# Optimization experiments

Hardware: AMD Instinct MI355X
Metric: run time of the kernel (lower is better)

The kernel has to match this reference:

```python
import jax, jax.numpy as jnp
import numpy as np

B, S, D, F, O = 4, 2048, 1024, 4096, 1024
E, NS, K = 4, 2, 2  # routed experts, shared experts, topk


def setup_inputs() -> dict:
    key = jax.random.key(0)
    ks = jax.random.split(key, 6)
    def w(k, shape, fan_in):
        return jax.random.normal(k, shape, jnp.float32) * (fan_in ** -0.5)
    return {
        "x": jax.random.normal(ks[0], (B, S, D), jnp.float32),
        "gate_w": w(ks[1], (D, E), D),
        "gate_b": jnp.zeros((E,), jnp.float32),
        "sw1": w(ks[2], (NS, D, F), D),  # shared experts, first linear
        "sb1": jnp.zeros((NS, F), jnp.float32),
        "sw2": w(ks[3], (NS, F, O), F),
        "sb2": jnp.zeros((NS, O), jnp.float32),
        "rw1": w(ks[4], (E, D, F), D),   # routed experts, first linear
        "rb1": jnp.zeros((E, F), jnp.float32),
        "rw2": w(ks[5], (E, F, O), F),
        "rb2": jnp.zeros((E, O), jnp.float32),
    }


def reference(x, gate_w, gate_b, sw1, sb1, sw2, sb2, rw1, rb1, rw2, rb2):
    # Gating (eval mode: no noise)
    weights = jax.nn.softmax(x @ gate_w + gate_b, axis=-1)      # [B,S,E]
    topk_w, topk_i = jax.lax.top_k(weights, K)                  # [B,S,K]

    # Shared experts: average of NS expert MLPs
    sh = jax.nn.relu(jnp.einsum('bsd,ndf->bsnf', x, sw1) + sb1)
    shared = (jnp.einsum('bsnf,nfo->bsno', sh, sw2) + sb2).sum(axis=2) / NS  # [B,S,O]

    # Routed experts: every expert applied densely, then one-hot-select topk.
    # Original computes expert(expanded_x) where expanded_x repeats x K times;
    # the result is identical per copy, so compute once per expert and gather.
    rh = jax.nn.relu(jnp.einsum('bsd,edf->bsef', x, rw1) + rb1)  # [B,S,E,F]
    eo = jnp.einsum('bsef,efo->bseo', rh, rw2) + rb2             # [B,S,E,O]
    gathered = jnp.take_along_axis(eo, topk_i[..., None], axis=2)  # [B,S,K,O]
    routed = (gathered * topk_w[..., None]).sum(axis=2)          # [B,S,O]

    return shared + routed
```

## Files before the change

### kernel.cpp

```cpp
#include <hip/hip_runtime.h>

typedef __bf16 bf16_t;
typedef __bf16 bf16x8 __attribute__((ext_vector_type(8)));
typedef float f32x4 __attribute__((ext_vector_type(4)));

constexpr int Tn = 4 * 2048;
constexpr int Dd = 1024;
constexpr int Ff = 4096;
constexpr int Oo = 1024;
constexpr int NEXP = 6;

__device__ __forceinline__ float ldin(const void* p, size_t i, int isf32) {
    return isf32 ? ((const float*)p)[i] : (float)((const bf16_t*)p)[i];
}

__global__ void detect_kernel(const unsigned int* __restrict__ xw, int* __restrict__ flag) {
    __shared__ int cnt;
    if (threadIdx.x == 0) cnt = 0;
    __syncthreads();
    int c = 0;
    for (int i = threadIdx.x; i < 16384; i += 256) {
        unsigned w = xw[i];
        if (((w >> 7) & 0xFFu) == 0xFFu) ++c;
    }
    atomicAdd(&cnt, c);
    __syncthreads();
    if (threadIdx.x == 0) flag[0] = (cnt >= 4) ? 1 : 0;
}

__global__ void cvt_x_kernel(const void* __restrict__ x, const int* __restrict__ flag,
                             bf16_t* __restrict__ xb) {
    int f = flag[0];
    size_t i = (size_t)blockIdx.x * 256 + threadIdx.x;
    xb[i] = (bf16_t)ldin(x, i, f);
}

__global__ void cvt_transpose_kernel(const void* __restrict__ src, size_t eofs,
                                     const int* __restrict__ flag,
                                     bf16_t* __restrict__ dst, int R, int C) {
    __shared__ bf16_t tile[32][33];
    int f = flag[0];
    int c0 = blockIdx.x * 32, r0 = blockIdx.y * 32;
    int tx = threadIdx.x, ty = threadIdx.y;
    #pragma unroll
    for (int i = 0; i < 32; i += 8)
        tile[ty + i][tx] = (bf16_t)ldin(src, eofs + (size_t)(r0 + ty + i) * C + c0 + tx, f);
    __syncthreads();
    #pragma unroll
    for (int i = 0; i < 32; i += 8)
        dst[(size_t)(c0 + ty + i) * R + r0 + tx] = tile[tx][ty + i];
}

__global__ void gate_kernel(const void* __restrict__ x, const void* __restrict__ gw,
                            const void* __restrict__ gb, const int* __restrict__ flag,
                            float* __restrict__ coef) {
    int f = flag[0];
    int t = blockIdx.x;
    int lane = threadIdx.x;
    float a0 = 0.f, a1 = 0.f, a2 = 0.f, a3 = 0.f;
    for (int d = lane; d < Dd; d += 64) {
        float xv = ldin(x, (size_t)t * Dd + d, f);
        a0 += xv * ldin(gw, (size_t)d * 4 + 0, f);
        a1 += xv * ldin(gw, (size_t)d * 4 + 1, f);
        a2 += xv * ldin(gw, (size_t)d * 4 + 2, f);
        a3 += xv * ldin(gw, (size_t)d * 4 + 3, f);
    }
    #pragma unroll
    for (int off = 32; off; off >>= 1) {
        a0 += __shfl_xor(a0, off);
        a1 += __shfl_xor(a1, off);
        a2 += __shfl_xor(a2, off);
        a3 += __shfl_xor(a3, off);
    }
    if (lane == 0) {
        float l[4] = {a0 + ldin(gb, 0, f), a1 + ldin(gb, 1, f),
                      a2 + ldin(gb, 2, f), a3 + ldin(gb, 3, f)};
        float mx = fmaxf(fmaxf(l[0], l[1]), fmaxf(l[2], l[3]));
        float e[4], s = 0.f;
        #pragma unroll
        for (int i = 0; i < 4; ++i) { e[i] = expf(l[i] - mx); s += e[i]; }
        float w[4];
        #pragma unroll
        for (int i = 0; i < 4; ++i) w[i] = e[i] / s;
        int i0 = 0;
        for (int i = 1; i < 4; ++i) if (w[i] > w[i0]) i0 = i;
        int i1 = -1;
        for (int i = 0; i < 4; ++i) { if (i == i0) continue; if (i1 < 0 || w[i] > w[i1]) i1 = i; }
        float c[8] = {0.5f, 0.5f, 0.f, 0.f, 0.f, 0.f, 0.f, 0.f};
        c[2 + i0] = w[i0];
        c[2 + i1] = w[i1];
        float* dst = coef + (size_t)t * 8;
        #pragma unroll
        for (int k = 0; k < 8; ++k) dst[k] = c[k];
    }
}

__global__ void init_acc_kernel(const float* __restrict__ coef, const void* __restrict__ sb2,
                                const void* __restrict__ rb2, const int* __restrict__ flag,
                                float* __restrict__ acc) {
    int f = flag[0];
    size_t idx = (size_t)blockIdx.x * 256 + threadIdx.x;
    int t = (int)(idx >> 10);
    int o = (int)(idx & 1023);
    const float* c = coef + (size_t)t * 8;
    float v = c[0] * ldin(sb2, o, f) + c[1] * ldin(sb2, Oo + o, f)
            + c[2] * ldin(rb2, o, f) + c[3] * ldin(rb2, Oo + o, f)
            + c[4] * ldin(rb2, 2 * Oo + o, f) + c[5] * ldin(rb2, 3 * Oo + o, f);
    acc[idx] = v;
}

__global__ void convert_kernel(const float* __restrict__ acc, const int* __restrict__ flag,
                               void* __restrict__ out) {
    int f = flag[0];
    size_t idx = (size_t)blockIdx.x * 256 + threadIdx.x;
    float v = acc[idx];
    if (v != v) v = 333.0f;
    if (f) ((float*)out)[idx] = v;
    else   ((bf16_t*)out)[idx] = (bf16_t)v;
}

template <int MODE, int BN_, int WM_>
__launch_bounds__(512, 2)
__global__ void gemm_kernel(const bf16_t* __restrict__ A, const bf16_t* __restrict__ Bt,
                            int M, int N, int K,
                            const void* __restrict__ bias, size_t b1_e,
                            const int* __restrict__ flag,
                            const float* __restrict__ coef,
                            bf16_t* __restrict__ obf, float* __restrict__ oacc) {
    constexpr int BM = 256, BK = 64;
    constexpr int WN_ = 8 / WM_;
    constexpr int NI = 16 / WM_;
    constexpr int NJ = BN_ / (WN_ * 16);
    constexpr int NIH = NI / 2;
    constexpr int NJH = NJ / 2;
    constexpr int ALOADS = 4;
    constexpr int BLOADS = BN_ / 64;
    constexpr int TOT = ALOADS + BLOADS;

    __shared__ __align__(16) bf16_t Al[2][BM * BK];
    __shared__ __align__(16) bf16_t Bl[2][BN_ * BK];

    const int tid = threadIdx.x;
    const int lane = tid & 63;
    const int wave = tid >> 6;
    const int wm = wave / WN_;
    const int wn = wave % WN_;
    const int l15 = lane & 15;
    const int l4 = lane >> 4;
    const int r7 = l15 & 7;

    const int gx = gridDim.x;
    const int nwg = gx * gridDim.y;
    const int id = blockIdx.y * gx + blockIdx.x;
    const int cpx = nwg >> 3;
    const int sid = (id & 7) * cpx + (id >> 3);
    const int bm = (sid % gx) * BM;
    const int bn = (sid / gx) * BN_;

    const int nK = K / BK;

    auto stage = [&](int t, int b) {
        const int k0 = t * BK;
        #pragma unroll
        for (int it = 0; it < ALOADS; ++it) {
            int q = it * 512 + tid;
            int row = q >> 3, c8 = q & 7;
            int k8 = c8 ^ (row & 7);
            const bf16_t* g = A + (size_t)(bm + row) * K + k0 + k8 * 8;
            __builtin_amdgcn_global_load_lds(
                (const __attribute__((address_space(1))) unsigned int*)g,
                (__attribute__((address_space(3))) unsigned int*)(&Al[b][q * 8]), 16, 0, 0);
        }
        #pragma unroll
        for (int it = 0; it < BLOADS; ++it) {
            int q = it * 512 + tid;
            int row = q >> 3, c8 = q & 7;
            int k8 = c8 ^ (row & 7);
            const bf16_t* g = Bt + (size_t)(bn + row) * K + k0 + k8 * 8;
            __builtin_amdgcn_global_load_lds(
                (const __attribute__((address_space(1))) unsigned int*)g,
                (__attribute__((address_space(3))) unsigned int*)(&Bl[b][q * 8]), 16, 0, 0);
        }
    };

    f32x4 acc[NI][NJ] = {};

    stage(0, 0);
    if (nK > 1) {
        stage(1, 1);
        if constexpr (TOT == 8) asm volatile("s_waitcnt vmcnt(8)" ::: "memory");
        else                    asm volatile("s_waitcnt vmcnt(6)" ::: "memory");
    } else {
        asm volatile("s_waitcnt vmcnt(0)" ::: "memory");
    }
    __builtin_amdgcn_sched_barrier(0);
    __builtin_amdgcn_s_barrier();
    __builtin_amdgcn_sched_barrier(0);

    const int a_off0 = ((l4 + 0) ^ r7) * 8;
    const int a_off1 = ((l4 + 4) ^ r7) * 8;
    const int arow = wm * (NI * 16) + l15;
    const int brow = wn * (NJ * 16) + l15;

    for (int t = 0; t < nK; ++t) {
        const bf16_t* __restrict__ Ab = Al[t & 1];
        const bf16_t* __restrict__ Bb = Bl[t & 1];
        bf16x8 bfv[NJ][2];
        bf16x8 af[NIH][2];
        #pragma unroll
        for (int j = 0; j < NJ; ++j) {
            bfv[j][0] = *(const bf16x8*)&Bb[(brow + j * 16) * BK + a_off0];
            bfv[j][1] = *(const bf16x8*)&Bb[(brow + j * 16) * BK + a_off1];
        }
        #pragma unroll
        for (int ih = 0; ih < 2; ++ih) {
            #pragma unroll
            for (int i = 0; i < NIH; ++i) {
                af[i][0] = *(const bf16x8*)&Ab[(arow + (ih * NIH + i) * 16) * BK + a_off0];
                af[i][1] = *(const bf16x8*)&Ab[(arow + (ih * NIH + i) * 16) * BK + a_off1];
            }
            #pragma unroll
            for (int jh = 0; jh < 2; ++jh) {
                __builtin_amdgcn_s_setprio(1);
                #pragma unroll
                for (int kx = 0; kx < 2; ++kx)
                    #pragma unroll
                    for (int i = 0; i < NIH; ++i)
                        #pragma unroll
                        for (int j = 0; j < NJH; ++j)
                            acc[ih * NIH + i][jh * NJH + j] =
                                __builtin_amdgcn_mfma_f32_16x16x32_bf16(
                                    af[i][kx], bfv[jh * NJH + j][kx],
                                    acc[ih * NIH + i][jh * NJH + j], 0, 0, 0);
                __builtin_amdgcn_s_setprio(0);
            }
        }
        if (t + 1 < nK) {
            asm volatile("s_waitcnt lgkmcnt(0)" ::: "memory");
            __builtin_amdgcn_sched_barrier(0);
            __builtin_amdgcn_s_barrier();
            __builtin_amdgcn_sched_barrier(0);
            if (t + 2 < nK) {
                stage(t + 2, t & 1);
                if constexpr (TOT == 8) asm volatile("s_waitcnt vmcnt(8)" ::: "memory");
                else                    asm volatile("s_waitcnt vmcnt(6)" ::: "memory");
            } else {
                asm volatile("s_waitcnt vmcnt(0)" ::: "memory");
            }
            __builtin_amdgcn_sched_barrier(0);
            __builtin_amdgcn_s_barrier();
            __builtin_amdgcn_sched_barrier(0);
        }
    }

    if (MODE == 1) {
        const int isf32 = flag[0];
        float bz[NJ];
        #pragma unroll
        for (int j = 0; j < NJ; ++j)
            bz[j] = ldin(bias, b1_e + (size_t)(bn + wn * (NJ * 16) + j * 16 + l15), isf32);
        #pragma unroll
        for (int i = 0; i < NI; ++i) {
            #pragma unroll
            for (int r = 0; r < 4; ++r) {
                int m = bm + wm * (NI * 16) + i * 16 + l4 * 4 + r;
                float cf = coef[(size_t)m * 8];
                #pragma unroll
                for (int j = 0; j < NJ; ++j) {
                    float v = acc[i][j][r] + bz[j];
                    v = fmaxf(v, 0.f) * cf;
                    obf[(size_t)m * N + bn + wn * (NJ * 16) + j * 16 + l15] = (bf16_t)v;
                }
            }
        }
    } else {
        #pragma unroll
        for (int i = 0; i < NI; ++i) {
            #pragma unroll
            for (int r = 0; r < 4; ++r) {
                int m = bm + wm * (NI * 16) + i * 16 + l4 * 4 + r;
                float* orow = oacc + (size_t)m * N + bn + wn * (NJ * 16) + l15;
                #pragma unroll
                for (int j = 0; j < NJ; ++j)
                    orow[j * 16] += acc[i][j][r];
            }
        }
    }
}

extern "C" void kernel_launch(void* const* d_in, const int* in_sizes, int n_in,
                              void* d_out, int out_size, void* d_ws, size_t ws_size,
                              hipStream_t stream) {
    const void* x      = d_in[0];
    const void* gate_w = d_in[1];
    const void* gate_b = d_in[2];
    const void* sw1    = d_in[3];
    const void* sb1    = d_in[4];
    const void* sw2    = d_in[5];
    const void* sb2    = d_in[6];
    const void* rw1    = d_in[7];
    const void* rb1    = d_in[8];
    const void* rw2    = d_in[9];
    const void* rb2    = d_in[10];

    char* ws = (char*)d_ws;
    int* flag = (int*)ws;
    size_t off = 256;
    bf16_t* W1T = (bf16_t*)(ws + off); off += (size_t)Ff * Dd * sizeof(bf16_t);
    bf16_t* W2T = (bf16_t*)(ws + off); off += (size_t)Oo * Ff * sizeof(bf16_t);
    bf16_t* xb  = (bf16_t*)(ws + off); off += (size_t)Tn * Dd * sizeof(bf16_t);
    float* coef = (float*)(ws + off);  off += (size_t)Tn * 8 * sizeof(float);
    float* accb = (float*)(ws + off);  off += (size_t)Tn * Oo * sizeof(float);
    bf16_t* Hs  = (bf16_t*)(ws + off);
    size_t rem = (ws_size > off) ? (ws_size - off) : 0;
    long tcap = (long)(rem / ((size_t)Ff * sizeof(bf16_t)));
    int Tc = (int)((tcap / 256) * 256);
    if (Tc < 256) Tc = 256;
    if (Tc > Tn) Tc = Tn;

    detect_kernel<<<1, 256, 0, stream>>>((const unsigned int*)x, flag);
    cvt_x_kernel<<<(Tn * Dd) / 256, 256, 0, stream>>>(x, flag, xb);
    gate_kernel<<<Tn, 64, 0, stream>>>(x, gate_w, gate_b, flag, coef);
    init_acc_kernel<<<(Tn * Oo) / 256, 256, 0, stream>>>(coef, sb2, rb2, flag, accb);

    dim3 tb(32, 8);
    for (int j = 0; j < NEXP; ++j) {
        const void* w1 = (j < 2) ? sw1 : rw1;
        const void* w2 = (j < 2) ? sw2 : rw2;
        const void* b1 = (j < 2) ? sb1 : rb1;
        int je = (j < 2) ? j : (j - 2);
        size_t w1_e = (size_t)je * Dd * Ff;
        size_t w2_e = (size_t)je * Ff * Oo;
        size_t b1_e = (size_t)je * Ff;

        cvt_transpose_kernel<<<dim3(Ff / 32, Dd / 32), tb, 0, stream>>>(w1, w1_e, flag, W1T, Dd, Ff);
        cvt_transpose_kernel<<<dim3(Oo / 32, Ff / 32), tb, 0, stream>>>(w2, w2_e, flag, W2T, Ff, Oo);

        for (int tok0 = 0; tok0 < Tn; tok0 += Tc) {
            int tc = (Tn - tok0 < Tc) ? (Tn - tok0) : Tc;
            gemm_kernel<1, 256, 2><<<dim3(tc / 256, Ff / 256), 512, 0, stream>>>(
                xb + (size_t)tok0 * Dd, W1T, tc, Ff, Dd,
                b1, b1_e, flag, coef + (size_t)tok0 * 8 + j, Hs, nullptr);
            gemm_kernel<2, 128, 4><<<dim3(tc / 256, Oo / 128), 512, 0, stream>>>(
                Hs, W2T, tc, Oo, Ff, nullptr, 0, flag, nullptr, nullptr,
                accb + (size_t)tok0 * Oo);
        }
    }

    convert_kernel<<<(Tn * Oo) / 256, 256, 0, stream>>>(accb, flag, d_out);
}
```

Before: 1.402 ms.

## Interleave half-tile global-to-LDS prefetch with MFMA quadrants in GEMM main loop

Splits each K-step into four MFMA quadrants and issues the next B tile halves and the A tile halves for two steps ahead between quadrants, with barriers around each. This replaces the single bulk prefetch after compute, so global loads overlap compute and LDS reads are spread out. It also removes the XCD-aware block-id swizzle and maps blocks directly from blockIdx, which may hurt L2 locality across chiplets. The barrier-heavy schedule and hardcoded vmcnt counts assume specific load counts per stage.

```diff
diff --git a/kernel.cpp b/kernel.cpp
--- a/kernel.cpp
+++ b/kernel.cpp
@@ -129,13 +129,12 @@
                             bf16_t* __restrict__ obf, float* __restrict__ oacc) {
     constexpr int BM = 256, BK = 64;
     constexpr int WN_ = 8 / WM_;
-    constexpr int NI = 16 / WM_;
+    constexpr int NI = BM / (WM_ * 16);
     constexpr int NJ = BN_ / (WN_ * 16);
     constexpr int NIH = NI / 2;
     constexpr int NJH = NJ / 2;
-    constexpr int ALOADS = 4;
-    constexpr int BLOADS = BN_ / 64;
-    constexpr int TOT = ALOADS + BLOADS;
+    constexpr int LPH_B = BN_ / 128;
+    constexpr int BHALF = BN_ * 4;
 
     __shared__ __align__(16) bf16_t Al[2][BM * BK];
     __shared__ __align__(16) bf16_t Bl[2][BN_ * BK];
@@ -149,50 +148,45 @@
     const int l4 = lane >> 4;
     const int r7 = l15 & 7;
 
-    const int gx = gridDim.x;
-    const int nwg = gx * gridDim.y;
-    const int id = blockIdx.y * gx + blockIdx.x;
-    const int cpx = nwg >> 3;
-    const int sid = (id & 7) * cpx + (id >> 3);
-    const int bm = (sid % gx) * BM;
-    const int bn = (sid / gx) * BN_;
-
+    const int bm = blockIdx.x * BM;
+    const int bn = blockIdx.y * BN_;
     const int nK = K / BK;
 
-    auto stage = [&](int t, int b) {
-        const int k0 = t * BK;
-        #pragma unroll
-        for (int it = 0; it < ALOADS; ++it) {
+    auto stageA = [&](int x, int h, int db) {
+        const int k0 = x * BK;
+        #pragma unroll
+        for (int it = 0; it < 2; ++it) {
             int q = it * 512 + tid;
-            int row = q >> 3, c8 = q & 7;
-            int k8 = c8 ^ (row & 7);
+            int row = (q >> 3) + h * 128;
+            int k8 = (q & 7) ^ ((q >> 3) & 7);
             const bf16_t* g = A + (size_t)(bm + row) * K + k0 + k8 * 8;
             __builtin_amdgcn_global_load_lds(
                 (const __attribute__((address_space(1))) unsigned int*)g,
-                (__attribute__((address_space(3))) unsigned int*)(&Al[b][q * 8]), 16, 0, 0);
-        }
-        #pragma unroll
-        for (int it = 0; it < BLOADS; ++it) {
+                (__attribute__((address_space(3))) unsigned int*)(&Al[db][(h * 1024 + q) * 8]),
+                16, 0, 0);
+        }
+    };
+    auto stageB = [&](int x, int h, int db) {
+        const int k0 = x * BK;
+        #pragma unroll
+        for (int it = 0; it < LPH_B; ++it) {
             int q = it * 512 + tid;
-            int row = q >> 3, c8 = q & 7;
-            int k8 = c8 ^ (row & 7);
+            int row = (q >> 3) + h * (BN_ / 2);
+            int k8 = (q & 7) ^ ((q >> 3) & 7);
             const bf16_t* g = Bt + (size_t)(bn + row) * K + k0 + k8 * 8;
             __builtin_amdgcn_global_load_lds(
                 (const __attribute__((address_space(1))) unsigned int*)g,
-                (__attribute__((address_space(3))) unsigned int*)(&Bl[b][q * 8]), 16, 0, 0);
+                (__attribute__((address_space(3))) unsigned int*)(&Bl[db][(h * BHALF + q) * 8]),
+                16, 0, 0);
         }
     };
 
     f32x4 acc[NI][NJ] = {};
 
-    stage(0, 0);
-    if (nK > 1) {
-        stage(1, 1);
-        if constexpr (TOT == 8) asm volatile("s_waitcnt vmcnt(8)" ::: "memory");
-        else                    asm volatile("s_waitcnt vmcnt(6)" ::: "memory");
-    } else {
-        asm volatile("s_waitcnt vmcnt(0)" ::: "memory");
-    }
+    stageA(0, 0, 0); stageA(0, 1, 0);
+    stageB(0, 0, 0); stageB(0, 1, 0);
+    stageA(1, 0, 1); stageA(1, 1, 1);
+    asm volatile("s_waitcnt vmcnt(4)" ::: "memory");
     __builtin_amdgcn_sched_barrier(0);
     __builtin_amdgcn_s_barrier();
     __builtin_amdgcn_sched_barrier(0);
@@ -203,54 +197,82 @@
     const int brow = wn * (NJ * 16) + l15;
 
     for (int t = 0; t < nK; ++t) {
-        const bf16_t* __restrict__ Ab = Al[t & 1];
-        const bf16_t* __restrict__ Bb = Bl[t & 1];
-        bf16x8 bfv[NJ][2];
-        bf16x8 af[NIH][2];
-        #pragma unroll
-        for (int j = 0; j < NJ; ++j) {
-            bfv[j][0] = *(const bf16x8*)&Bb[(brow + j * 16) * BK + a_off0];
-            bfv[j][1] = *(const bf16x8*)&Bb[(brow + j * 16) * BK + a_off1];
-        }
-        #pragma unroll
-        for (int ih = 0; ih < 2; ++ih) {
-            #pragma unroll
-            for (int i = 0; i < NIH; ++i) {
-                af[i][0] = *(const bf16x8*)&Ab[(arow + (ih * NIH + i) * 16) * BK + a_off0];
-                af[i][1] = *(const bf16x8*)&Ab[(arow + (ih * NIH + i) * 16) * BK + a_off1];
-            }
-            #pragma unroll
-            for (int jh = 0; jh < 2; ++jh) {
-                __builtin_amdgcn_s_setprio(1);
-                #pragma unroll
-                for (int kx = 0; kx < 2; ++kx)
-                    #pragma unroll
-                    for (int i = 0; i < NIH; ++i)
-                        #pragma unroll
-                        for (int j = 0; j < NJH; ++j)
-                            acc[ih * NIH + i][jh * NJH + j] =
-                                __builtin_amdgcn_mfma_f32_16x16x32_bf16(
-                                    af[i][kx], bfv[jh * NJH + j][kx],
-                                    acc[ih * NIH + i][jh * NJH + j], 0, 0, 0);
-                __builtin_amdgcn_s_setprio(0);
-            }
-        }
-        if (t + 1 < nK) {
-            asm volatile("s_waitcnt lgkmcnt(0)" ::: "memory");
+        const int b = t & 1;
+        const bf16_t* __restrict__ Ab = Al[b];
+        const bf16_t* __restrict__ Bb = Bl[b];
+        const bool s1 = (t + 1 < nK);
+        const bool s2 = (t + 2 < nK);
+
+        bf16x8 af[NI][2];
+        bf16x8 bv[NJH][2];
+
+#define QUAD(IH, JH)                                                              \
+    __builtin_amdgcn_s_setprio(1);                                                \
+    _Pragma("unroll")                                                             \
+    for (int kx = 0; kx < 2; ++kx)                                                \
+        _Pragma("unroll")                                                         \
+        for (int i = 0; i < NIH; ++i)                                             \
+            _Pragma("unroll")                                                     \
+            for (int j = 0; j < NJH; ++j)                                         \
+                acc[(IH) * NIH + i][(JH) * NJH + j] =                             \
+                    __builtin_amdgcn_mfma_f32_16x16x32_bf16(                      \
+                        af[(IH) * NIH + i][kx], bv[j][kx],                        \
+                        acc[(IH) * NIH + i][(JH) * NJH + j], 0, 0, 0);            \
+    __builtin_amdgcn_s_setprio(0);
+
+        #pragma unroll
+        for (int i = 0; i < NIH; ++i) {
+            af[i][0] = *(const bf16x8*)&Ab[(arow + i * 16) * BK + a_off0];
+            af[i][1] = *(const bf16x8*)&Ab[(arow + i * 16) * BK + a_off1];
+        }
+        #pragma unroll
+        for (int j = 0; j < NJH; ++j) {
+            bv[j][0] = *(const bf16x8*)&Bb[(brow + j * 16) * BK + a_off0];
+            bv[j][1] = *(const bf16x8*)&Bb[(brow + j * 16) * BK + a_off1];
+        }
+        if (s1) stageB(t + 1, 0, b ^ 1);
+        __builtin_amdgcn_s_barrier();
+        asm volatile("s_waitcnt lgkmcnt(0)" ::: "memory");
+        __builtin_amdgcn_sched_barrier(0);
+        QUAD(0, 0)
+        __builtin_amdgcn_s_barrier();
+
+        #pragma unroll
+        for (int i = 0; i < NIH; ++i) {
+            af[NIH + i][0] = *(const bf16x8*)&Ab[(arow + (NIH + i) * 16) * BK + a_off0];
+            af[NIH + i][1] = *(const bf16x8*)&Ab[(arow + (NIH + i) * 16) * BK + a_off1];
+        }
+        if (s1) stageB(t + 1, 1, b ^ 1);
+        __builtin_amdgcn_s_barrier();
+        asm volatile("s_waitcnt lgkmcnt(0)" ::: "memory");
+        __builtin_amdgcn_sched_barrier(0);
+        QUAD(1, 0)
+        __builtin_amdgcn_s_barrier();
+
+        #pragma unroll
+        for (int j = 0; j < NJH; ++j) {
+            bv[j][0] = *(const bf16x8*)&Bb[(brow + (NJH + j) * 16) * BK + a_off0];
+            bv[j][1] = *(const bf16x8*)&Bb[(brow + (NJH + j) * 16) * BK + a_off1];
+        }
+        if (s2) stageA(t + 2, 0, b);
+        __builtin_amdgcn_s_barrier();
+        asm volatile("s_waitcnt lgkmcnt(0)" ::: "memory");
+        __builtin_amdgcn_sched_barrier(0);
+        QUAD(0, 1)
+        __builtin_amdgcn_s_barrier();
+
+        if (s2) stageA(t + 2, 1, b);
+        __builtin_amdgcn_s_barrier();
+        QUAD(1, 1)
+
+        if (s1) {
+            __builtin_amdgcn_s_barrier();
+            if (s2) { asm volatile("s_waitcnt vmcnt(4)" ::: "memory"); }
+            else    { asm volatile("s_waitcnt vmcnt(0)" ::: "memory"); }
             __builtin_amdgcn_sched_barrier(0);
             __builtin_amdgcn_s_barrier();
-            __builtin_amdgcn_sched_barrier(0);
-            if (t + 2 < nK) {
-                stage(t + 2, t & 1);
-                if constexpr (TOT == 8) asm volatile("s_waitcnt vmcnt(8)" ::: "memory");
-                else                    asm volatile("s_waitcnt vmcnt(6)" ::: "memory");
-            } else {
-                asm volatile("s_waitcnt vmcnt(0)" ::: "memory");
-            }
-            __builtin_amdgcn_sched_barrier(0);
-            __builtin_amdgcn_s_barrier();
-            __builtin_amdgcn_sched_barrier(0);
-        }
+        }
+#undef QUAD
     }
 
     if (MODE == 1) {
```

After: 1.319 ms. 1.06x faster.
